# Kernel optimization log

Hardware: AMD Instinct MI355X
Metric: run time of the kernel (lower is better)

## Reference

```python
import jax, jax.numpy as jnp
import numpy as np

ALPHA = 100.0
EPS = 1e-12  # torch F.normalize eps


def setup_inputs() -> dict:
    key = jax.random.key(0)
    k1, k2 = jax.random.split(key)
    N, C, H, W, K = 32, 512, 56, 56, 64
    x = jax.random.normal(k1, (N, C, H, W), dtype=jnp.float32)
    centroids = jax.random.uniform(k2, (K, C), dtype=jnp.float32)  # torch.rand
    # _init_params: conv weight/bias are independent params initialized from centroids
    conv_w = 2.0 * ALPHA * centroids                      # (K, C), 1x1 conv kernel
    conv_b = -ALPHA * jnp.linalg.norm(centroids, axis=1)  # (K,)
    return {"x": x, "centroids": centroids, "conv_w": conv_w, "conv_b": conv_b}


def reference(x, centroids, conv_w, conv_b):
    N, C, H, W = x.shape
    K = centroids.shape[0]
    P = H * W
    xf = x.reshape(N, C, P)  # local descriptors, (N, C, P)

    # 1x1 conv == per-pixel linear; softmax over clusters
    logits = jnp.einsum('ncp,kc->nkp', xf, conv_w) + conv_b[None, :, None]
    a = jax.nn.softmax(logits, axis=1)  # (N, K, P)

    # Faithful to original: centroids.view(C, K) is a row-major RESHAPE, not transpose
    cent_r = jnp.reshape(centroids, (C, K))  # (C, K)

    # Algebraic rewrite of sum_p a[n,k,p] * (x[n,c,p] - cent_r[c,k]):
    # avoids the (N, C, K, P) intermediate entirely.
    vlad = jnp.einsum('ncp,nkp->nck', xf, a) - cent_r[None] * a.sum(-1)[:, None, :]  # (N, C, K)

    # intra-normalization over dim=2 (clusters), as in original code
    vlad = vlad / jnp.clip(jnp.linalg.norm(vlad, axis=2, keepdims=True), EPS)
    vlad = vlad.reshape(N, C * K)
    vlad = vlad / jnp.clip(jnp.linalg.norm(vlad, axis=1, keepdims=True), EPS)
    return vlad
```

## Files before the change

### kernel.cpp

```cpp
#include <hip/hip_runtime.h>
#include <math.h>

#define N_DIM 32
#define C_DIM 512
#define K_DIM 64
#define P_DIM 3136


__global__ __launch_bounds__(256) void k_prep(const float* __restrict__ conv_w,
                                              float* __restrict__ wt) {
    const int b = blockIdx.x, t = threadIdx.x;
#pragma unroll
    for (int r = 0; r < 4; ++r) {
        int idx = b * 1024 + r * 256 + t;
        int c = idx >> 6, k = idx & 63;
        wt[idx] = conv_w[k * C_DIM + c];
    }
}

__global__ __launch_bounds__(256) void k_logits(const float* __restrict__ x,
                                                const float* __restrict__ wt,
                                                const float* __restrict__ bias,
                                                float* __restrict__ a_t,
                                                float* __restrict__ asum_part) {
    __shared__ float xs[32][224];
    __shared__ float wsh[32][64];
    __shared__ float asl[4][64];
    const int tid = threadIdx.x;
    const int n  = blockIdx.y;
    const int pblk = blockIdx.x;
    const int p0 = pblk * 224;
    const int tp = tid >> 3;
    const int tk = tid & 7;

    float acc[7][8];
    {
        float4 b0 = *(const float4*)(bias + tk * 8);
        float4 b1 = *(const float4*)(bias + tk * 8 + 4);
        float br[8] = {b0.x, b0.y, b0.z, b0.w, b1.x, b1.y, b1.z, b1.w};
#pragma unroll
        for (int i = 0; i < 7; ++i)
#pragma unroll
            for (int j = 0; j < 8; ++j) acc[i][j] = br[j];
    }

    const float* xn = x + (size_t)n * C_DIM * P_DIM + p0;

    float4 xv[7], wv[2];
#pragma unroll
    for (int i = 0; i < 7; ++i) {
        int f = tid + 256 * i;
        xv[i] = *(const float4*)(xn + (size_t)(f / 56) * P_DIM + (f % 56) * 4);
    }
    wv[0] = *(const float4*)(wt + (tid >> 4) * K_DIM + (tid & 15) * 4);
    wv[1] = *(const float4*)(wt + ((tid + 256) >> 4) * K_DIM + (tid & 15) * 4);

    for (int cc = 0; cc < C_DIM; cc += 32) {
        __syncthreads();
#pragma unroll
        for (int i = 0; i < 7; ++i) {
            int f = tid + 256 * i;
            *(float4*)&xs[f / 56][(f % 56) * 4] = xv[i];
        }
        *(float4*)&wsh[tid >> 4][(tid & 15) * 4] = wv[0];
        *(float4*)&wsh[(tid + 256) >> 4][(tid & 15) * 4] = wv[1];
        __syncthreads();

        if (cc + 32 < C_DIM) {
            const float* xc = xn + (size_t)(cc + 32) * P_DIM;
#pragma unroll
            for (int i = 0; i < 7; ++i) {
                int f = tid + 256 * i;
                xv[i] = *(const float4*)(xc + (size_t)(f / 56) * P_DIM + (f % 56) * 4);
            }
            const float* wc = wt + (cc + 32) * K_DIM;
            wv[0] = *(const float4*)(wc + (tid >> 4) * K_DIM + (tid & 15) * 4);
            wv[1] = *(const float4*)(wc + ((tid + 256) >> 4) * K_DIM + (tid & 15) * 4);
        }

#pragma unroll 8
        for (int c = 0; c < 32; ++c) {
            float xr[7];
#pragma unroll
            for (int i = 0; i < 7; ++i) xr[i] = xs[c][tp + 32 * i];
            float4 w0 = *(const float4*)&wsh[c][tk * 8];
            float4 w1 = *(const float4*)&wsh[c][tk * 8 + 4];
            float wr[8] = {w0.x, w0.y, w0.z, w0.w, w1.x, w1.y, w1.z, w1.w};
#pragma unroll
            for (int i = 0; i < 7; ++i)
#pragma unroll
                for (int j = 0; j < 8; ++j)
                    acc[i][j] = fmaf(xr[i], wr[j], acc[i][j]);
        }
    }

    float sk[8] = {0.f, 0.f, 0.f, 0.f, 0.f, 0.f, 0.f, 0.f};
#pragma unroll
    for (int i = 0; i < 7; ++i) {
        float m = acc[i][0];
#pragma unroll
        for (int j = 1; j < 8; ++j) m = fmaxf(m, acc[i][j]);
        m = fmaxf(m, __shfl_xor(m, 1));
        m = fmaxf(m, __shfl_xor(m, 2));
        m = fmaxf(m, __shfl_xor(m, 4));
        float e[8], s = 0.f;
#pragma unroll
        for (int j = 0; j < 8; ++j) { e[j] = __expf(acc[i][j] - m); s += e[j]; }
        s += __shfl_xor(s, 1);
        s += __shfl_xor(s, 2);
        s += __shfl_xor(s, 4);
        const float inv = 1.0f / s;
        float* ap = a_t + ((size_t)n * P_DIM + p0 + tp + 32 * i) * K_DIM + tk * 8;
        float4 o0, o1;
        o0.x = e[0] * inv; o0.y = e[1] * inv; o0.z = e[2] * inv; o0.w = e[3] * inv;
        o1.x = e[4] * inv; o1.y = e[5] * inv; o1.z = e[6] * inv; o1.w = e[7] * inv;
        *(float4*)ap = o0;
        *(float4*)(ap + 4) = o1;
        sk[0] += o0.x; sk[1] += o0.y; sk[2] += o0.z; sk[3] += o0.w;
        sk[4] += o1.x; sk[5] += o1.y; sk[6] += o1.z; sk[7] += o1.w;
    }
#pragma unroll
    for (int j = 0; j < 8; ++j) {
        sk[j] += __shfl_xor(sk[j], 8);
        sk[j] += __shfl_xor(sk[j], 16);
        sk[j] += __shfl_xor(sk[j], 32);
    }
    const int lane = tid & 63, wv_ = tid >> 6;
    if (lane < 8) {
#pragma unroll
        for (int j = 0; j < 8; ++j) asl[wv_][lane * 8 + j] = sk[j];
    }
    __syncthreads();
    if (tid < 64)
        asum_part[((size_t)n * 14 + pblk) * K_DIM + tid] =
            asl[0][tid] + asl[1][tid] + asl[2][tid] + asl[3][tid];
}

__global__ __launch_bounds__(256) void k_red(const float* __restrict__ asum_part,
                                             float* __restrict__ asum) {
    const int idx = blockIdx.x * 256 + threadIdx.x;
    const int n = idx >> 6, k = idx & 63;
    float s = 0.f;
#pragma unroll
    for (int b = 0; b < 14; ++b)
        s += asum_part[((size_t)n * 14 + b) * K_DIM + k];
    asum[idx] = s;
}

__global__ __launch_bounds__(128) void k_gemm2(const float* __restrict__ x,
                                               const float* __restrict__ a_t,
                                               float* __restrict__ part,
                                               int pslice) {
    __shared__ float xs[16][132];
    __shared__ float as[16][64];
    const int tid = threadIdx.x;
    const int c0 = blockIdx.x * 128;
    const int n  = blockIdx.y;
    const int s  = blockIdx.z;
    const int p0 = s * pslice;
    const int tc = tid >> 3;
    const int tk = tid & 7;

    float acc[8][8];
#pragma unroll
    for (int i = 0; i < 8; ++i)
#pragma unroll
        for (int j = 0; j < 8; ++j) acc[i][j] = 0.f;

    const float* xb = x + ((size_t)n * C_DIM + c0) * P_DIM + p0;
    const float* ab = a_t + ((size_t)n * P_DIM + p0) * K_DIM;

    float4 xv[4], av[2];
#pragma unroll
    for (int i = 0; i < 4; ++i) {
        int f = tid + 128 * i;
        xv[i] = *(const float4*)(xb + (size_t)(f >> 2) * P_DIM + (f & 3) * 4);
    }
#pragma unroll
    for (int i = 0; i < 2; ++i) {
        int f = tid + 128 * i;
        av[i] = *(const float4*)(ab + (size_t)(f >> 4) * K_DIM + (f & 15) * 4);
    }

    for (int pb = 0; pb < pslice; pb += 16) {
        __syncthreads();
#pragma unroll
        for (int i = 0; i < 4; ++i) {
            int f = tid + 128 * i;
            int c = f >> 2, pe = (f & 3) * 4;
            xs[pe + 0][c] = xv[i].x;
            xs[pe + 1][c] = xv[i].y;
            xs[pe + 2][c] = xv[i].z;
            xs[pe + 3][c] = xv[i].w;
        }
#pragma unroll
        for (int i = 0; i < 2; ++i) {
            int f = tid + 128 * i;
            *(float4*)&as[f >> 4][(f & 15) * 4] = av[i];
        }
        __syncthreads();

        if (pb + 16 < pslice) {
            const float* xc = xb + pb + 16;
            const float* ac = ab + (size_t)(pb + 16) * K_DIM;
#pragma unroll
            for (int i = 0; i < 4; ++i) {
                int f = tid + 128 * i;
                xv[i] = *(const float4*)(xc + (size_t)(f >> 2) * P_DIM + (f & 3) * 4);
            }
#pragma unroll
            for (int i = 0; i < 2; ++i) {
                int f = tid + 128 * i;
                av[i] = *(const float4*)(ac + (size_t)(f >> 4) * K_DIM + (f & 15) * 4);
            }
        }

#pragma unroll 4
        for (int p = 0; p < 16; ++p) {
            float4 x0 = *(const float4*)&xs[p][tc * 8];
            float4 x1 = *(const float4*)&xs[p][tc * 8 + 4];
            float4 a0 = *(const float4*)&as[p][tk * 8];
            float4 a1 = *(const float4*)&as[p][tk * 8 + 4];
            float xr[8] = {x0.x, x0.y, x0.z, x0.w, x1.x, x1.y, x1.z, x1.w};
            float ar[8] = {a0.x, a0.y, a0.z, a0.w, a1.x, a1.y, a1.z, a1.w};
#pragma unroll
            for (int i = 0; i < 8; ++i)
#pragma unroll
                for (int j = 0; j < 8; ++j)
                    acc[i][j] = fmaf(xr[i], ar[j], acc[i][j]);
        }
    }

    float* po = part + (((size_t)s * N_DIM + n) * C_DIM + c0 + tc * 8) * K_DIM + tk * 8;
#pragma unroll
    for (int i = 0; i < 8; ++i) {
        float4 o0, o1;
        o0.x = acc[i][0]; o0.y = acc[i][1]; o0.z = acc[i][2]; o0.w = acc[i][3];
        o1.x = acc[i][4]; o1.y = acc[i][5]; o1.z = acc[i][6]; o1.w = acc[i][7];
        *(float4*)&po[(size_t)i * K_DIM] = o0;
        *(float4*)&po[(size_t)i * K_DIM + 4] = o1;
    }
}

template <int S>
__global__ __launch_bounds__(256) void k_intra(const float* __restrict__ part,
                                               const float* __restrict__ cent,
                                               const float* __restrict__ asum,
                                               float* __restrict__ out,
                                               float* __restrict__ ssb) {
    const int w = (blockIdx.x * 256 + threadIdx.x) >> 6;
    const int lane = threadIdx.x & 63;
    const int n = w >> 9;
    const int c = w & 511;
    const size_t off = ((size_t)n * C_DIM + c) * K_DIM + lane;
    const size_t stride = (size_t)N_DIM * C_DIM * K_DIM;

    float v = 0.f;
#pragma unroll
    for (int s = 0; s < S; ++s) v += part[s * stride + off];
    v -= cent[c * K_DIM + lane] * asum[n * K_DIM + lane];

    float ss = v * v;
#pragma unroll
    for (int o = 32; o > 0; o >>= 1) ss += __shfl_xor(ss, o);

    const float denom = fmaxf(sqrtf(ss), 1e-12f);
    out[off] = v / denom;
    if (lane == 0) ssb[w] = ss / (denom * denom);
}

__global__ __launch_bounds__(256) void k_gsum(const float* __restrict__ ssb,
                                              float* __restrict__ gsum) {
    const int n = blockIdx.x, t = threadIdx.x;
    float s = ssb[n * C_DIM + t] + ssb[n * C_DIM + t + 256];
    __shared__ float red[256];
    red[t] = s;
    __syncthreads();
    for (int o = 128; o > 0; o >>= 1) {
        if (t < o) red[t] += red[t + o];
        __syncthreads();
    }
    if (t == 0) gsum[n] = red[0];
}

__global__ __launch_bounds__(256) void k_final(float* __restrict__ out,
                                               const float* __restrict__ gsum) {
    const size_t i = (size_t)blockIdx.x * 256 + threadIdx.x;
    const int n = (int)(i >> 15);
    const float g = sqrtf(gsum[n]);
    out[i] = out[i] / fmaxf(g, 1e-12f);
}

extern "C" void kernel_launch(void* const* d_in, const int* in_sizes, int n_in,
                              void* d_out, int out_size, void* d_ws, size_t ws_size,
                              hipStream_t stream) {
    const float* x      = (const float*)d_in[0];
    const float* cent   = (const float*)d_in[1];
    const float* conv_w = (const float*)d_in[2];
    const float* conv_b = (const float*)d_in[3];

    float* ws    = (float*)d_ws;
    float* wt    = ws;
    float* a_t   = wt + 32768;
    float* asum  = a_t + (size_t)N_DIM * P_DIM * K_DIM;
    float* apart = asum + 2048;
    float* gsum  = apart + 28672;
    float* ssb   = gsum + 32;
    float* part  = ssb + 16384;
    float* out   = (float*)d_out;

    const size_t base_f = (size_t)(part - ws);
    const size_t cxk = (size_t)N_DIM * C_DIM * K_DIM;
    int S = 14;
    if (ws_size < (base_f + 14 * cxk) * 4) S = 7;
    if (ws_size < (base_f + 7 * cxk) * 4) S = 2;
    const int pslice = P_DIM / S;

    hipLaunchKernelGGL(k_prep,   dim3(32),        dim3(256), 0, stream, conv_w, wt);
    hipLaunchKernelGGL(k_logits, dim3(14, 32),    dim3(256), 0, stream, x, wt, conv_b, a_t, apart);
    hipLaunchKernelGGL(k_red,    dim3(8),         dim3(256), 0, stream, apart, asum);
    hipLaunchKernelGGL(k_gemm2,  dim3(4, 32, S),  dim3(128), 0, stream, x, a_t, part, pslice);
    if (S == 14)
        hipLaunchKernelGGL(k_intra<14>, dim3(4096), dim3(256), 0, stream, part, cent, asum, out, ssb);
    else if (S == 7)
        hipLaunchKernelGGL(k_intra<7>,  dim3(4096), dim3(256), 0, stream, part, cent, asum, out, ssb);
    else
        hipLaunchKernelGGL(k_intra<2>,  dim3(4096), dim3(256), 0, stream, part, cent, asum, out, ssb);
    hipLaunchKernelGGL(k_gsum,   dim3(32),        dim3(256), 0, stream, ssb, gsum);
    hipLaunchKernelGGL(k_final,  dim3(4096),      dim3(256), 0, stream, out, gsum);
}
```

Baseline: 506.5 us.

## Retile logits kernel to 64-pixel blocks with LDS-staged coalesced softmax stores

The logits kernel moves from 224-pixel tiles with 256 threads to 64-pixel tiles with 128 threads, raising the grid from 14x32 to 49x32 blocks so more of the GPU is occupied. Softmax outputs are staged through shared memory and written to a_t as contiguous float4 rows instead of scattered per-thread stores. The second GEMM changes its per-thread micro-tile from 8x8 to 16 channels by 4 clusters, which changes how LDS reads are shaped. Trade-offs: each block reuses weights over fewer pixels, and k_red now sums more partial rows.

New measurement: 554.3 us. +9.4%, slower.

```diff
diff --git a/kernel.cpp b/kernel.cpp
--- a/kernel.cpp
+++ b/kernel.cpp
@@ -5,6 +5,7 @@
 #define C_DIM 512
 #define K_DIM 64
 #define P_DIM 3136
+#define PT 49
 
 
 __global__ __launch_bounds__(256) void k_prep(const float* __restrict__ conv_w,
@@ -18,76 +19,76 @@
     }
 }
 
-__global__ __launch_bounds__(256) void k_logits(const float* __restrict__ x,
+__global__ __launch_bounds__(128) void k_logits(const float* __restrict__ x,
                                                 const float* __restrict__ wt,
                                                 const float* __restrict__ bias,
                                                 float* __restrict__ a_t,
                                                 float* __restrict__ asum_part) {
-    __shared__ float xs[32][224];
-    __shared__ float wsh[32][64];
-    __shared__ float asl[4][64];
+    __shared__ float smem[4096 + 128];
+    float (*xs)[64]  = (float (*)[64])smem;
+    float (*wsh)[64] = (float (*)[64])(smem + 2048);
+    float* tb  = smem;
+    float* asl = smem + 4096;
+
     const int tid = threadIdx.x;
     const int n  = blockIdx.y;
-    const int pblk = blockIdx.x;
-    const int p0 = pblk * 224;
+    const int pt = blockIdx.x;
+    const int p0 = pt * 64;
     const int tp = tid >> 3;
     const int tk = tid & 7;
 
-    float acc[7][8];
+    float acc[4][8];
     {
         float4 b0 = *(const float4*)(bias + tk * 8);
         float4 b1 = *(const float4*)(bias + tk * 8 + 4);
         float br[8] = {b0.x, b0.y, b0.z, b0.w, b1.x, b1.y, b1.z, b1.w};
 #pragma unroll
-        for (int i = 0; i < 7; ++i)
+        for (int i = 0; i < 4; ++i)
 #pragma unroll
             for (int j = 0; j < 8; ++j) acc[i][j] = br[j];
     }
 
     const float* xn = x + (size_t)n * C_DIM * P_DIM + p0;
 
-    float4 xv[7], wv[2];
-#pragma unroll
-    for (int i = 0; i < 7; ++i) {
-        int f = tid + 256 * i;
-        xv[i] = *(const float4*)(xn + (size_t)(f / 56) * P_DIM + (f % 56) * 4);
-    }
-    wv[0] = *(const float4*)(wt + (tid >> 4) * K_DIM + (tid & 15) * 4);
-    wv[1] = *(const float4*)(wt + ((tid + 256) >> 4) * K_DIM + (tid & 15) * 4);
+    float4 xv[4], wv[4];
+#pragma unroll
+    for (int i = 0; i < 4; ++i) {
+        int f = tid + 128 * i;
+        xv[i] = *(const float4*)(xn + (size_t)(f >> 4) * P_DIM + (f & 15) * 4);
+        wv[i] = *(const float4*)(wt + (f >> 4) * K_DIM + (f & 15) * 4);
+    }
 
     for (int cc = 0; cc < C_DIM; cc += 32) {
         __syncthreads();
 #pragma unroll
-        for (int i = 0; i < 7; ++i) {
-            int f = tid + 256 * i;
-            *(float4*)&xs[f / 56][(f % 56) * 4] = xv[i];
-        }
-        *(float4*)&wsh[tid >> 4][(tid & 15) * 4] = wv[0];
-        *(float4*)&wsh[(tid + 256) >> 4][(tid & 15) * 4] = wv[1];
+        for (int i = 0; i < 4; ++i) {
+            int f = tid + 128 * i;
+            *(float4*)&xs[f >> 4][(f & 15) * 4] = xv[i];
+            *(float4*)&wsh[f >> 4][(f & 15) * 4] = wv[i];
+        }
         __syncthreads();
 
         if (cc + 32 < C_DIM) {
             const float* xc = xn + (size_t)(cc + 32) * P_DIM;
-#pragma unroll
-            for (int i = 0; i < 7; ++i) {
-                int f = tid + 256 * i;
-                xv[i] = *(const float4*)(xc + (size_t)(f / 56) * P_DIM + (f % 56) * 4);
+            const float* wc = wt + (cc + 32) * K_DIM;
+#pragma unroll
+            for (int i = 0; i < 4; ++i) {
+                int f = tid + 128 * i;
+                xv[i] = *(const float4*)(xc + (size_t)(f >> 4) * P_DIM + (f & 15) * 4);
+                wv[i] = *(const float4*)(wc + (f >> 4) * K_DIM + (f & 15) * 4);
             }
-            const float* wc = wt + (cc + 32) * K_DIM;
-            wv[0] = *(const float4*)(wc + (tid >> 4) * K_DIM + (tid & 15) * 4);
-            wv[1] = *(const float4*)(wc + ((tid + 256) >> 4) * K_DIM + (tid & 15) * 4);
         }
 
 #pragma unroll 8
         for (int c = 0; c < 32; ++c) {
-            float xr[7];
-#pragma unroll
-            for (int i = 0; i < 7; ++i) xr[i] = xs[c][tp + 32 * i];
+            float xr[4];
+#pragma unroll
+            for (int i = 0; i < 4; ++i) xr[i] = xs[c][tp + 16 * i];
             float4 w0 = *(const float4*)&wsh[c][tk * 8];
             float4 w1 = *(const float4*)&wsh[c][tk * 8 + 4];
             float wr[8] = {w0.x, w0.y, w0.z, w0.w, w1.x, w1.y, w1.z, w1.w};
 #pragma unroll
-            for (int i = 0; i < 7; ++i)
+            for (int i = 0; i < 4; ++i)
 #pragma unroll
                 for (int j = 0; j < 8; ++j)
                     acc[i][j] = fmaf(xr[i], wr[j], acc[i][j]);
@@ -96,28 +97,22 @@
 
     float sk[8] = {0.f, 0.f, 0.f, 0.f, 0.f, 0.f, 0.f, 0.f};
 #pragma unroll
-    for (int i = 0; i < 7; ++i) {
+    for (int i = 0; i < 4; ++i) {
         float m = acc[i][0];
 #pragma unroll
         for (int j = 1; j < 8; ++j) m = fmaxf(m, acc[i][j]);
         m = fmaxf(m, __shfl_xor(m, 1));
         m = fmaxf(m, __shfl_xor(m, 2));
         m = fmaxf(m, __shfl_xor(m, 4));
-        float e[8], s = 0.f;
-#pragma unroll
-        for (int j = 0; j < 8; ++j) { e[j] = __expf(acc[i][j] - m); s += e[j]; }
+        float s = 0.f;
+#pragma unroll
+        for (int j = 0; j < 8; ++j) { acc[i][j] = __expf(acc[i][j] - m); s += acc[i][j]; }
         s += __shfl_xor(s, 1);
         s += __shfl_xor(s, 2);
         s += __shfl_xor(s, 4);
         const float inv = 1.0f / s;
-        float* ap = a_t + ((size_t)n * P_DIM + p0 + tp + 32 * i) * K_DIM + tk * 8;
-        float4 o0, o1;
-        o0.x = e[0] * inv; o0.y = e[1] * inv; o0.z = e[2] * inv; o0.w = e[3] * inv;
-        o1.x = e[4] * inv; o1.y = e[5] * inv; o1.z = e[6] * inv; o1.w = e[7] * inv;
-        *(float4*)ap = o0;
-        *(float4*)(ap + 4) = o1;
-        sk[0] += o0.x; sk[1] += o0.y; sk[2] += o0.z; sk[3] += o0.w;
-        sk[4] += o1.x; sk[5] += o1.y; sk[6] += o1.z; sk[7] += o1.w;
+#pragma unroll
+        for (int j = 0; j < 8; ++j) { acc[i][j] *= inv; sk[j] += acc[i][j]; }
     }
 #pragma unroll
     for (int j = 0; j < 8; ++j) {
@@ -125,15 +120,29 @@
         sk[j] += __shfl_xor(sk[j], 16);
         sk[j] += __shfl_xor(sk[j], 32);
     }
-    const int lane = tid & 63, wv_ = tid >> 6;
+
+    __syncthreads();
+#pragma unroll
+    for (int i = 0; i < 4; ++i) {
+        float* t = tb + (tp + 16 * i) * K_DIM + tk * 8;
+        *(float4*)t       = make_float4(acc[i][0], acc[i][1], acc[i][2], acc[i][3]);
+        *(float4*)(t + 4) = make_float4(acc[i][4], acc[i][5], acc[i][6], acc[i][7]);
+    }
+    const int lane = tid & 63, wvi = tid >> 6;
     if (lane < 8) {
 #pragma unroll
-        for (int j = 0; j < 8; ++j) asl[wv_][lane * 8 + j] = sk[j];
+        for (int j = 0; j < 8; ++j) asl[wvi * 64 + lane * 8 + j] = sk[j];
     }
     __syncthreads();
+
+    float* ab = a_t + ((size_t)n * P_DIM + p0) * K_DIM;
+#pragma unroll
+    for (int r = 0; r < 8; ++r) {
+        int f = tid + 128 * r;
+        *(float4*)(ab + 4 * f) = *(const float4*)(tb + 4 * f);
+    }
     if (tid < 64)
-        asum_part[((size_t)n * 14 + pblk) * K_DIM + tid] =
-            asl[0][tid] + asl[1][tid] + asl[2][tid] + asl[3][tid];
+        asum_part[((size_t)n * PT + pt) * K_DIM + tid] = asl[tid] + asl[64 + tid];
 }
 
 __global__ __launch_bounds__(256) void k_red(const float* __restrict__ asum_part,
@@ -142,8 +151,8 @@
     const int n = idx >> 6, k = idx & 63;
     float s = 0.f;
 #pragma unroll
-    for (int b = 0; b < 14; ++b)
-        s += asum_part[((size_t)n * 14 + b) * K_DIM + k];
+    for (int b = 0; b < PT; ++b)
+        s += asum_part[((size_t)n * PT + b) * K_DIM + k];
     asum[idx] = s;
 }
 
@@ -158,14 +167,14 @@
     const int n  = blockIdx.y;
     const int s  = blockIdx.z;
     const int p0 = s * pslice;
-    const int tc = tid >> 3;
-    const int tk = tid & 7;
-
-    float acc[8][8];
-#pragma unroll
-    for (int i = 0; i < 8; ++i)
-#pragma unroll
-        for (int j = 0; j < 8; ++j) acc[i][j] = 0.f;
+    const int tc  = tid >> 4;
+    const int tk4 = tid & 15;
+
+    float acc[16][4];
+#pragma unroll
+    for (int i = 0; i < 16; ++i)
+#pragma unroll
+        for (int j = 0; j < 4; ++j) acc[i][j] = 0.f;
 
     const float* xb = x + ((size_t)n * C_DIM + c0) * P_DIM + p0;
     const float* ab = a_t + ((size_t)n * P_DIM + p0) * K_DIM;
@@ -217,28 +226,28 @@
 
 #pragma unroll 4
         for (int p = 0; p < 16; ++p) {
-            float4 x0 = *(const float4*)&xs[p][tc * 8];
-            float4 x1 = *(const float4*)&xs[p][tc * 8 + 4];
-            float4 a0 = *(const float4*)&as[p][tk * 8];
-            float4 a1 = *(const float4*)&as[p][tk * 8 + 4];
-            float xr[8] = {x0.x, x0.y, x0.z, x0.w, x1.x, x1.y, x1.z, x1.w};
-            float ar[8] = {a0.x, a0.y, a0.z, a0.w, a1.x, a1.y, a1.z, a1.w};
-#pragma unroll
-            for (int i = 0; i < 8; ++i)
-#pragma unroll
-                for (int j = 0; j < 8; ++j)
+            float4 a4 = *(const float4*)&as[p][tk4 * 4];
+            float ar[4] = {a4.x, a4.y, a4.z, a4.w};
+            float xr[16];
+#pragma unroll
+            for (int q = 0; q < 4; ++q) {
+                float4 xq = *(const float4*)&xs[p][tc * 16 + q * 4];
+                xr[q * 4 + 0] = xq.x; xr[q * 4 + 1] = xq.y;
+                xr[q * 4 + 2] = xq.z; xr[q * 4 + 3] = xq.w;
+            }
+#pragma unroll
+            for (int i = 0; i < 16; ++i)
+#pragma unroll
+                for (int j = 0; j < 4; ++j)
                     acc[i][j] = fmaf(xr[i], ar[j], acc[i][j]);
         }
     }
 
-    float* po = part + (((size_t)s * N_DIM + n) * C_DIM + c0 + tc * 8) * K_DIM + tk * 8;
-#pragma unroll
-    for (int i = 0; i < 8; ++i) {
-        float4 o0, o1;
-        o0.x = acc[i][0]; o0.y = acc[i][1]; o0.z = acc[i][2]; o0.w = acc[i][3];
-        o1.x = acc[i][4]; o1.y = acc[i][5]; o1.z = acc[i][6]; o1.w = acc[i][7];
-        *(float4*)&po[(size_t)i * K_DIM] = o0;
-        *(float4*)&po[(size_t)i * K_DIM + 4] = o1;
+    float* po = part + (((size_t)s * N_DIM + n) * C_DIM + c0 + tc * 16) * K_DIM + tk4 * 4;
+#pragma unroll
+    for (int i = 0; i < 16; ++i) {
+        *(float4*)&po[(size_t)i * K_DIM] =
+            make_float4(acc[i][0], acc[i][1], acc[i][2], acc[i][3]);
     }
 }
 
@@ -304,7 +313,7 @@
     float* a_t   = wt + 32768;
     float* asum  = a_t + (size_t)N_DIM * P_DIM * K_DIM;
     float* apart = asum + 2048;
-    float* gsum  = apart + 28672;
+    float* gsum  = apart + (size_t)N_DIM * PT * K_DIM;
     float* ssb   = gsum + 32;
     float* part  = ssb + 16384;
     float* out   = (float*)d_out;
@@ -317,7 +326,7 @@
     const int pslice = P_DIM / S;
 
     hipLaunchKernelGGL(k_prep,   dim3(32),        dim3(256), 0, stream, conv_w, wt);
-    hipLaunchKernelGGL(k_logits, dim3(14, 32),    dim3(256), 0, stream, x, wt, conv_b, a_t, apart);
+    hipLaunchKernelGGL(k_logits, dim3(PT, 32),    dim3(128), 0, stream, x, wt, conv_b, a_t, apart);
     hipLaunchKernelGGL(k_red,    dim3(8),         dim3(256), 0, stream, apart, asum);
     hipLaunchKernelGGL(k_gemm2,  dim3(4, 32, S),  dim3(128), 0, stream, x, a_t, part, pslice);
     if (S == 14)
```
